# Performance work log

Measured on AMD Instinct MI355X. Metric: run time of the kernel, lower is better.

Reference implementation:

```python
import jax, jax.numpy as jnp
import numpy as np

T, H, E, I, K = 1024, 2048, 32, 1024, 2  # tokens, hidden, experts, intermediate (per rank), top_k


def setup_inputs() -> dict:
    key = jax.random.key(0)
    k0, k1, k2, k3 = jax.random.split(key, 4)
    s = 0.02  # weight init scale
    return {
        "hidden_states": jax.random.normal(k0, (T, H), jnp.float32),
        "w_qkv": jax.random.normal(k1, (3 * E, H), jnp.float32) * s,   # router query_key_value weight
        "w1": jax.random.normal(k2, (E, 2 * I, H), jnp.float32) * s,   # gate/up projection per expert
        "w2": jax.random.normal(k3, (E, H, I), jnp.float32) * s,       # down projection per expert
    }


def _router_logits(x, w_qkv):
    # ParallelAttention_router: per-token attention over the expert axis.
    mix = x @ w_qkv.T                      # [T, 3E]
    q, k, v = jnp.split(mix, 3, axis=-1)   # each [T, E]
    q = q.astype(jnp.float32)
    k = k.astype(jnp.float32)
    v = v.astype(jnp.float32)
    # attn[t, e, f] = softmax_f(q[t, e] * k[t, f])
    attn = jax.nn.softmax(q[:, :, None] * k[:, None, :], axis=-1)  # [T, E, E]
    return jnp.einsum('tef,tf->te', attn, v)                        # [T, E]


def reference(hidden_states, w_qkv, w1, w2):
    n_tok = hidden_states.shape[0]
    logits = _router_logits(hidden_states, w_qkv)                   # [T, E]
    top_logits, topk_ids = jax.lax.top_k(logits, K)                 # [T, K]
    topk_w = jax.nn.softmax(top_logits.astype(jnp.float32), axis=-1)  # renormalize=False -> plain softmax over top-k
    # Dense combine weights: zero for non-selected experts (honors top-k sparsity in math).
    combine = jnp.zeros((n_tok, E), jnp.float32).at[
        jnp.arange(n_tok)[:, None], topk_ids].add(topk_w)           # [T, E]
    # Expert MLP: SiLU-gated FFN (fused_experts contract: w1 -> [gate; up], w2 -> down).
    gate_up = jnp.einsum('th,eih->tei', hidden_states, w1)          # [T, E, 2I]
    gate, up = jnp.split(gate_up, 2, axis=-1)                       # each [T, E, I]
    h = jax.nn.silu(gate) * up * combine[:, :, None]                # fold combine weight in early
    out = jnp.einsum('tei,ehi->th', h, w2)                          # [T, H]
    return out.astype(hidden_states.dtype)
```

## Files before the change

### kernel.cpp

```cpp
#include <hip/hip_runtime.h>
#include <hip/hip_bf16.h>
#include <math.h>

#define TT 1024
#define HH 2048
#define EE 32
#define II 1024
#define BK2 128
#define SA2 136
#define TS2 (128 * SA2)
#define KSP 32
#define MB 64

typedef __attribute__((ext_vector_type(8))) short bf16x8;
typedef __attribute__((ext_vector_type(8))) unsigned short ushort8;
typedef __attribute__((ext_vector_type(4))) float f32x4;

__device__ __forceinline__ unsigned short f2b(float f) {
    union { float f; unsigned u; } c; c.f = f;
    unsigned r = c.u + 0x7FFFu + ((c.u >> 16) & 1u);
    return (unsigned short)(r >> 16);
}
__device__ __forceinline__ float b2f(unsigned short u) {
    union { unsigned u; float f; } c; c.u = ((unsigned)u) << 16;
    return c.f;
}
__device__ __forceinline__ unsigned cvtpk(float lo, float hi) {
    unsigned r;
    asm("v_cvt_pk_bf16_f32 %0, %1, %2" : "=v"(r) : "v"(lo), "v"(hi));
    return r;
}
__device__ __forceinline__ ushort8 pack8(float4 a, float4 b) {
    union { unsigned u[4]; ushort8 s; } cv;
    cv.u[0] = cvtpk(a.x, a.y); cv.u[1] = cvtpk(a.z, a.w);
    cv.u[2] = cvtpk(b.x, b.y); cv.u[3] = cvtpk(b.z, b.w);
    return cv.s;
}

__global__ __launch_bounds__(256) void k_mix(const float* __restrict__ x,
                                             const float* __restrict__ wqkv,
                                             float* __restrict__ mixp,
                                             unsigned short* __restrict__ xb) {
    __shared__ float xs[MB][68];
    __shared__ float ws_[96][68];
    const int tm0 = blockIdx.x * MB;
    const int k0 = blockIdx.y * 64;
    const int tid = threadIdx.x;
#pragma unroll
    for (int q = 0; q < 4; ++q) {
        int p = tid + q * 256;
        int row = p >> 4, c4 = (p & 15) * 4;
        *(float4*)&xs[row][c4] = *(const float4*)(x + (size_t)(tm0 + row) * HH + k0 + c4);
    }
#pragma unroll
    for (int q = 0; q < 6; ++q) {
        int p = tid + q * 256;
        int row = p >> 4, c4 = (p & 15) * 4;
        *(float4*)&ws_[row][c4] = *(const float4*)(wqkv + (size_t)row * HH + k0 + c4);
    }
    __syncthreads();
#pragma unroll
    for (int q = 0; q < 2; ++q) {
        int p = tid + q * 256;
        int row = p >> 3, c8 = (p & 7) * 8;
        float4 lo = *(const float4*)&xs[row][c8];
        float4 hi = *(const float4*)&xs[row][c8 + 4];
        *(ushort8*)(xb + (size_t)(tm0 + row) * HH + k0 + c8) = pack8(lo, hi);
    }
    const int tg = tid >> 4, cg = tid & 15;
    float acc[4][6];
#pragma unroll
    for (int i = 0; i < 4; ++i)
#pragma unroll
        for (int c = 0; c < 6; ++c) acc[i][c] = 0.f;
    for (int k = 0; k < 64; k += 4) {
        float4 xv[4], wv[6];
#pragma unroll
        for (int i = 0; i < 4; ++i) xv[i] = *(const float4*)&xs[tg * 4 + i][k];
#pragma unroll
        for (int c = 0; c < 6; ++c) wv[c] = *(const float4*)&ws_[cg * 6 + c][k];
#pragma unroll
        for (int i = 0; i < 4; ++i)
#pragma unroll
            for (int c = 0; c < 6; ++c)
                acc[i][c] += xv[i].x * wv[c].x + xv[i].y * wv[c].y +
                             xv[i].z * wv[c].z + xv[i].w * wv[c].w;
    }
    float* dst = mixp + ((size_t)blockIdx.y * TT + tm0) * 96;
#pragma unroll
    for (int i = 0; i < 4; ++i)
#pragma unroll
        for (int c = 0; c < 6; ++c)
            dst[(tg * 4 + i) * 96 + cg * 6 + c] = acc[i][c];
}

__global__ void k_router_attn(const float* __restrict__ mixp,
                              int* __restrict__ cnt,
                              int* __restrict__ tok_list,
                              float* __restrict__ wgt_list) {
    const int t = blockIdx.x;
    __shared__ float mrow[96];
    __shared__ float lg[EE];
    const int tid = threadIdx.x;
    if (tid < 96) {
        float s = 0.f;
        for (int sp = 0; sp < KSP; ++sp)
            s += mixp[((size_t)sp * TT + t) * 96 + tid];
        mrow[tid] = s;
    }
    __syncthreads();
    if (tid < EE) {
        float q = mrow[tid];
        float m = -1e30f;
        for (int f = 0; f < EE; ++f) m = fmaxf(m, q * mrow[32 + f]);
        float s = 0.f, a = 0.f;
        for (int f = 0; f < EE; ++f) {
            float ex = expf(q * mrow[32 + f] - m);
            s += ex;
            a += ex * mrow[64 + f];
        }
        lg[tid] = a / s;
    }
    __syncthreads();
    if (tid == 0) {
        int b0 = 0; float v0 = lg[0];
        for (int e2 = 1; e2 < EE; ++e2)
            if (lg[e2] > v0) { v0 = lg[e2]; b0 = e2; }
        int b1 = -1; float v1 = -1e30f;
        for (int e2 = 0; e2 < EE; ++e2)
            if (e2 != b0 && lg[e2] > v1) { v1 = lg[e2]; b1 = e2; }
        float ex = expf(v1 - v0);
        float w0 = 1.f / (1.f + ex);
        float w1 = ex / (1.f + ex);
        int p0 = atomicAdd(&cnt[b0], 1);
        tok_list[b0 * TT + p0] = t * 2 + 0;
        wgt_list[b0 * TT + p0] = w0;
        int p1 = atomicAdd(&cnt[b1], 1);
        tok_list[b1 * TT + p1] = t * 2 + 1;
        wgt_list[b1 * TT + p1] = w1;
    }
}

__global__ __launch_bounds__(256, 2) void k_gemm1(
    const unsigned short* __restrict__ xb, const float* __restrict__ w1,
    const int* __restrict__ cnt, const int* __restrict__ tok_list,
    const float* __restrict__ wgt_list, unsigned short* __restrict__ act) {
    const int e = blockIdx.y;
    const int M = cnt[e];
    const int m0 = blockIdx.z * 128;
    if (m0 >= M) return;
    const int i0 = blockIdx.x * 64;

    __shared__ __align__(16) unsigned short As[TS2];
    __shared__ __align__(16) unsigned short Bs[TS2];
    __shared__ int ts[128];
    __shared__ float tw[128];

    const int tid = threadIdx.x;
    if (tid < 128) {
        int mr = m0 + tid;
        if (mr < M) {
            ts[tid] = tok_list[e * TT + mr];
            tw[tid] = wgt_list[e * TT + mr];
        } else { ts[tid] = -1; tw[tid] = 0.f; }
    }
    __syncthreads();

    const float* w1e = w1 + (size_t)e * (2 * II) * HH;
    const int wid = tid >> 6;
    const int lane = tid & 63;
    const int wm = wid >> 1, wn = wid & 1;
    const int fr = lane & 15;
    const int kg = lane >> 4;
    const int srow = tid >> 4;
    const int sc8 = (tid & 15) * 8;

    f32x4 acc[4][4];
#pragma unroll
    for (int i = 0; i < 4; ++i)
#pragma unroll
        for (int j = 0; j < 4; ++j) acc[i][j] = (f32x4){0.f, 0.f, 0.f, 0.f};

    ushort8 pa8[8];
    float4 pb[16];
    const ushort8 u8z = {0, 0, 0, 0, 0, 0, 0, 0};

#define G1_LOAD(kk)                                                              \
    do {                                                                         \
        const int kkv_ = (kk);                                                   \
        _Pragma("unroll")                                                        \
        for (int q = 0; q < 8; ++q) {                                            \
            int row = q * 16 + srow;                                             \
            int entry = ts[row];                                                 \
            pa8[q] = (entry >= 0)                                                \
                ? *(const ushort8*)(xb + (size_t)(entry >> 1) * HH + kkv_ + sc8) \
                : u8z;                                                           \
            int brow = (row < 64) ? (i0 + row) : (II + i0 + row - 64);           \
            const float* gpb_ = w1e + (size_t)brow * HH + kkv_ + sc8;            \
            pb[2 * q] = ((const float4*)gpb_)[0];                                \
            pb[2 * q + 1] = ((const float4*)gpb_)[1];                            \
        }                                                                        \
    } while (0)

#define G1_CVT()                                                                 \
    do {                                                                         \
        _Pragma("unroll")                                                        \
        for (int q = 0; q < 8; ++q) {                                            \
            int row = q * 16 + srow;                                             \
            *(ushort8*)&As[row * SA2 + sc8] = pa8[q];                            \
            *(ushort8*)&Bs[row * SA2 + sc8] = pack8(pb[2 * q], pb[2 * q + 1]);   \
        }                                                                        \
    } while (0)

    const int NS = HH / BK2;
    G1_LOAD(0);
    for (int s = 0; s < NS; ++s) {
        __syncthreads();
        G1_CVT();
        __syncthreads();
        if (s + 1 < NS) G1_LOAD((s + 1) * BK2);
#pragma unroll
        for (int kh = 0; kh < 4; ++kh) {
            const int kb = kh * 32 + kg * 8;
            bf16x8 a[4], b[4];
#pragma unroll
            for (int i = 0; i < 4; ++i)
                a[i] = *(const bf16x8*)&As[(wm * 64 + i * 16 + fr) * SA2 + kb];
#pragma unroll
            for (int j = 0; j < 4; ++j)
                b[j] = *(const bf16x8*)&Bs[(wn * 64 + j * 16 + fr) * SA2 + kb];
#pragma unroll
            for (int i = 0; i < 4; ++i)
#pragma unroll
                for (int j = 0; j < 4; ++j)
                    acc[i][j] = __builtin_amdgcn_mfma_f32_16x16x32_bf16(a[i], b[j], acc[i][j], 0, 0, 0);
        }
    }
#undef G1_LOAD
#undef G1_CVT

    unsigned short* upls = As;
    __syncthreads();
    if (wn == 1) {
#pragma unroll
        for (int mi = 0; mi < 4; ++mi)
#pragma unroll
            for (int reg = 0; reg < 4; ++reg) {
                int mrow = wm * 64 + mi * 16 + kg * 4 + reg;
#pragma unroll
                for (int ni = 0; ni < 4; ++ni)
                    upls[mrow * 64 + ni * 16 + fr] = f2b(acc[mi][ni][reg]);
            }
    }
    __syncthreads();
    if (wn == 0) {
#pragma unroll
        for (int mi = 0; mi < 4; ++mi)
#pragma unroll
            for (int reg = 0; reg < 4; ++reg) {
                int mrow = wm * 64 + mi * 16 + kg * 4 + reg;
                int entry = ts[mrow];
                if (entry < 0) continue;
                float w = tw[mrow];
                unsigned short* dst = act + (size_t)entry * II + i0;
#pragma unroll
                for (int ni = 0; ni < 4; ++ni) {
                    float g = acc[mi][ni][reg];
                    float u = b2f(upls[mrow * 64 + ni * 16 + fr]);
                    dst[ni * 16 + fr] = f2b((g / (1.f + __expf(-g))) * u * w);
                }
            }
    }
}

__global__ __launch_bounds__(256, 2) void k_gemm2(
    const unsigned short* __restrict__ act, const float* __restrict__ w2,
    const int* __restrict__ cnt, const int* __restrict__ tok_list,
    float* __restrict__ out) {
    const int e = blockIdx.y;
    const int M = cnt[e];
    const int m0 = blockIdx.z * 128;
    if (m0 >= M) return;
    const int n0 = blockIdx.x * 128;

    __shared__ __align__(16) unsigned short As[TS2];
    __shared__ __align__(16) unsigned short Bs[TS2];
    __shared__ int ts[128];

    const int tid = threadIdx.x;
    if (tid < 128) {
        int mr = m0 + tid;
        ts[tid] = (mr < M) ? tok_list[e * TT + mr] : -1;
    }
    __syncthreads();

    const float* w2e = w2 + (size_t)e * HH * II;
    const int wid = tid >> 6;
    const int lane = tid & 63;
    const int wm = wid >> 1, wn = wid & 1;
    const int fr = lane & 15;
    const int kg = lane >> 4;
    const int srow = tid >> 4;
    const int sc8 = (tid & 15) * 8;

    f32x4 acc[4][4];
#pragma unroll
    for (int i = 0; i < 4; ++i)
#pragma unroll
        for (int j = 0; j < 4; ++j) acc[i][j] = (f32x4){0.f, 0.f, 0.f, 0.f};

    ushort8 pa8[8];
    float4 pb[16];
    const ushort8 u8z = {0, 0, 0, 0, 0, 0, 0, 0};

#define G2_LOAD(kk)                                                              \
    do {                                                                         \
        const int kkv_ = (kk);                                                   \
        _Pragma("unroll")                                                        \
        for (int q = 0; q < 8; ++q) {                                            \
            int row = q * 16 + srow;                                             \
            int entry = ts[row];                                                 \
            pa8[q] = (entry >= 0)                                                \
                ? *(const ushort8*)(act + (size_t)entry * II + kkv_ + sc8)       \
                : u8z;                                                           \
            const float* gpb_ = w2e + (size_t)(n0 + row) * II + kkv_ + sc8;      \
            pb[2 * q] = ((const float4*)gpb_)[0];                                \
            pb[2 * q + 1] = ((const float4*)gpb_)[1];                            \
        }                                                                        \
    } while (0)

#define G2_CVT()                                                                 \
    do {                                                                         \
        _Pragma("unroll")                                                        \
        for (int q = 0; q < 8; ++q) {                                            \
            int row = q * 16 + srow;                                             \
            *(ushort8*)&As[row * SA2 + sc8] = pa8[q];                            \
            *(ushort8*)&Bs[row * SA2 + sc8] = pack8(pb[2 * q], pb[2 * q + 1]);   \
        }                                                                        \
    } while (0)

    const int NS = II / BK2;
    G2_LOAD(0);
    for (int s = 0; s < NS; ++s) {
        __syncthreads();
        G2_CVT();
        __syncthreads();
        if (s + 1 < NS) G2_LOAD((s + 1) * BK2);
#pragma unroll
        for (int kh = 0; kh < 4; ++kh) {
            const int kb = kh * 32 + kg * 8;
            bf16x8 a[4], b[4];
#pragma unroll
            for (int i = 0; i < 4; ++i)
                a[i] = *(const bf16x8*)&As[(wm * 64 + i * 16 + fr) * SA2 + kb];
#pragma unroll
            for (int j = 0; j < 4; ++j)
                b[j] = *(const bf16x8*)&Bs[(wn * 64 + j * 16 + fr) * SA2 + kb];
#pragma unroll
            for (int i = 0; i < 4; ++i)
#pragma unroll
                for (int j = 0; j < 4; ++j)
                    acc[i][j] = __builtin_amdgcn_mfma_f32_16x16x32_bf16(a[i], b[j], acc[i][j], 0, 0, 0);
        }
    }
#undef G2_LOAD
#undef G2_CVT

#pragma unroll
    for (int mi = 0; mi < 4; ++mi) {
#pragma unroll
        for (int reg = 0; reg < 4; ++reg) {
            int m = wm * 64 + mi * 16 + kg * 4 + reg;
            int entry = ts[m];
            if (entry < 0) continue;
            int t = entry >> 1;
            float* op = out + (size_t)t * HH + n0 + wn * 64;
#pragma unroll
            for (int ni = 0; ni < 4; ++ni)
                atomicAdd(&op[ni * 16 + fr], acc[mi][ni][reg]);
        }
    }
}

extern "C" void kernel_launch(void* const* d_in, const int* in_sizes, int n_in,
                              void* d_out, int out_size, void* d_ws, size_t ws_size,
                              hipStream_t stream) {
    const float* x    = (const float*)d_in[0];
    const float* wqkv = (const float*)d_in[1];
    const float* w1   = (const float*)d_in[2];
    const float* w2   = (const float*)d_in[3];
    float* out = (float*)d_out;

    char* ws = (char*)d_ws;
    float* mixp           = (float*)(ws);
    float* wgt_list       = (float*)(ws + 12582912);
    int*   tok_list       = (int*)  (ws + 12713984);
    int*   cnt            = (int*)  (ws + 12845056);
    unsigned short* xb    = (unsigned short*)(ws + 12845184);
    unsigned short* act   = (unsigned short*)(ws + 17039488);

    (void)hipMemsetAsync(cnt, 0, 128, stream);
    (void)hipMemsetAsync(out, 0, (size_t)out_size * sizeof(float), stream);

    k_mix<<<dim3(TT / MB, KSP), 256, 0, stream>>>(x, wqkv, mixp, xb);
    k_router_attn<<<TT, 128, 0, stream>>>(mixp, cnt, tok_list, wgt_list);
    k_gemm1<<<dim3(II / 64, EE, 8), 256, 0, stream>>>(xb, w1, cnt, tok_list, wgt_list, act);
    k_gemm2<<<dim3(HH / 128, EE, 8), 256, 0, stream>>>(act, w2, cnt, tok_list, out);
}
```

Before: 218.5 us.

## Use 512-thread blocks with BK=256 K-tiles and 2x4 warp layout in expert GEMMs

Both expert GEMM kernels now launch 512 threads (8 waves arranged 2x4) instead of 256, and the K-tile per stage doubles from 128 to 256, halving the number of sync/convert stages. Each wave computes a 64x32 sub-tile, which cuts accumulator registers per thread and doubles the waves per block that can hide the fp32 weight-load latency. The trade-off is doubled LDS per block (about 135 KB), which likely drops occupancy to one block per CU, plus more LDS A-fragment re-reads per MFMA. The gate/up epilogue is remapped to the new wave layout.

After: 231.4 us. 5.9% more time.

```diff
diff --git a/kernel.cpp b/kernel.cpp
--- a/kernel.cpp
+++ b/kernel.cpp
@@ -6,9 +6,9 @@
 #define HH 2048
 #define EE 32
 #define II 1024
-#define BK2 128
-#define SA2 136
-#define TS2 (128 * SA2)
+#define BK3 256
+#define SA3 264
+#define TS3 (128 * SA3)
 #define KSP 32
 #define MB 64
 
@@ -141,7 +141,7 @@
     }
 }
 
-__global__ __launch_bounds__(256, 2) void k_gemm1(
+__global__ __launch_bounds__(512, 2) void k_gemm1(
     const unsigned short* __restrict__ xb, const float* __restrict__ w1,
     const int* __restrict__ cnt, const int* __restrict__ tok_list,
     const float* __restrict__ wgt_list, unsigned short* __restrict__ act) {
@@ -151,8 +151,8 @@
     if (m0 >= M) return;
     const int i0 = blockIdx.x * 64;
 
-    __shared__ __align__(16) unsigned short As[TS2];
-    __shared__ __align__(16) unsigned short Bs[TS2];
+    __shared__ __align__(16) unsigned short As[TS3];
+    __shared__ __align__(16) unsigned short Bs[TS3];
     __shared__ int ts[128];
     __shared__ float tw[128];
 
@@ -169,17 +169,17 @@
     const float* w1e = w1 + (size_t)e * (2 * II) * HH;
     const int wid = tid >> 6;
     const int lane = tid & 63;
-    const int wm = wid >> 1, wn = wid & 1;
+    const int wm = wid >> 2, wn = wid & 3;
     const int fr = lane & 15;
     const int kg = lane >> 4;
-    const int srow = tid >> 4;
-    const int sc8 = (tid & 15) * 8;
-
-    f32x4 acc[4][4];
+    const int srow = tid >> 5;
+    const int sc8 = (tid & 31) * 8;
+
+    f32x4 acc[4][2];
 #pragma unroll
     for (int i = 0; i < 4; ++i)
 #pragma unroll
-        for (int j = 0; j < 4; ++j) acc[i][j] = (f32x4){0.f, 0.f, 0.f, 0.f};
+        for (int j = 0; j < 2; ++j) acc[i][j] = (f32x4){0.f, 0.f, 0.f, 0.f};
 
     ushort8 pa8[8];
     float4 pb[16];
@@ -207,32 +207,32 @@
         _Pragma("unroll")                                                        \
         for (int q = 0; q < 8; ++q) {                                            \
             int row = q * 16 + srow;                                             \
-            *(ushort8*)&As[row * SA2 + sc8] = pa8[q];                            \
-            *(ushort8*)&Bs[row * SA2 + sc8] = pack8(pb[2 * q], pb[2 * q + 1]);   \
+            *(ushort8*)&As[row * SA3 + sc8] = pa8[q];                            \
+            *(ushort8*)&Bs[row * SA3 + sc8] = pack8(pb[2 * q], pb[2 * q + 1]);   \
         }                                                                        \
     } while (0)
 
-    const int NS = HH / BK2;
+    const int NS = HH / BK3;
     G1_LOAD(0);
     for (int s = 0; s < NS; ++s) {
         __syncthreads();
         G1_CVT();
         __syncthreads();
-        if (s + 1 < NS) G1_LOAD((s + 1) * BK2);
-#pragma unroll
-        for (int kh = 0; kh < 4; ++kh) {
+        if (s + 1 < NS) G1_LOAD((s + 1) * BK3);
+#pragma unroll
+        for (int kh = 0; kh < 8; ++kh) {
             const int kb = kh * 32 + kg * 8;
-            bf16x8 a[4], b[4];
+            bf16x8 a[4], b[2];
 #pragma unroll
             for (int i = 0; i < 4; ++i)
-                a[i] = *(const bf16x8*)&As[(wm * 64 + i * 16 + fr) * SA2 + kb];
-#pragma unroll
-            for (int j = 0; j < 4; ++j)
-                b[j] = *(const bf16x8*)&Bs[(wn * 64 + j * 16 + fr) * SA2 + kb];
+                a[i] = *(const bf16x8*)&As[(wm * 64 + i * 16 + fr) * SA3 + kb];
+#pragma unroll
+            for (int j = 0; j < 2; ++j)
+                b[j] = *(const bf16x8*)&Bs[(wn * 32 + j * 16 + fr) * SA3 + kb];
 #pragma unroll
             for (int i = 0; i < 4; ++i)
 #pragma unroll
-                for (int j = 0; j < 4; ++j)
+                for (int j = 0; j < 2; ++j)
                     acc[i][j] = __builtin_amdgcn_mfma_f32_16x16x32_bf16(a[i], b[j], acc[i][j], 0, 0, 0);
         }
     }
@@ -241,39 +241,42 @@
 
     unsigned short* upls = As;
     __syncthreads();
-    if (wn == 1) {
+    if (wn >= 2) {
 #pragma unroll
         for (int mi = 0; mi < 4; ++mi)
 #pragma unroll
             for (int reg = 0; reg < 4; ++reg) {
-                int mrow = wm * 64 + mi * 16 + kg * 4 + reg;
-#pragma unroll
-                for (int ni = 0; ni < 4; ++ni)
-                    upls[mrow * 64 + ni * 16 + fr] = f2b(acc[mi][ni][reg]);
-            }
-    }
-    __syncthreads();
-    if (wn == 0) {
-#pragma unroll
-        for (int mi = 0; mi < 4; ++mi)
-#pragma unroll
-            for (int reg = 0; reg < 4; ++reg) {
-                int mrow = wm * 64 + mi * 16 + kg * 4 + reg;
-                int entry = ts[mrow];
-                if (entry < 0) continue;
-                float w = tw[mrow];
-                unsigned short* dst = act + (size_t)entry * II + i0;
-#pragma unroll
-                for (int ni = 0; ni < 4; ++ni) {
-                    float g = acc[mi][ni][reg];
-                    float u = b2f(upls[mrow * 64 + ni * 16 + fr]);
-                    dst[ni * 16 + fr] = f2b((g / (1.f + __expf(-g))) * u * w);
+                int m = wm * 64 + mi * 16 + kg * 4 + reg;
+#pragma unroll
+                for (int j = 0; j < 2; ++j) {
+                    int un = (wn - 2) * 32 + j * 16 + fr;
+                    upls[m * 64 + un] = f2b(acc[mi][j][reg]);
                 }
             }
     }
-}
-
-__global__ __launch_bounds__(256, 2) void k_gemm2(
+    __syncthreads();
+    if (wn < 2) {
+#pragma unroll
+        for (int mi = 0; mi < 4; ++mi)
+#pragma unroll
+            for (int reg = 0; reg < 4; ++reg) {
+                int m = wm * 64 + mi * 16 + kg * 4 + reg;
+                int entry = ts[m];
+                if (entry < 0) continue;
+                float w = tw[m];
+                unsigned short* dst = act + (size_t)entry * II + i0;
+#pragma unroll
+                for (int j = 0; j < 2; ++j) {
+                    int n = wn * 32 + j * 16 + fr;
+                    float g = acc[mi][j][reg];
+                    float u = b2f(upls[m * 64 + n]);
+                    dst[n] = f2b((g / (1.f + __expf(-g))) * u * w);
+                }
+            }
+    }
+}
+
+__global__ __launch_bounds__(512, 2) void k_gemm2(
     const unsigned short* __restrict__ act, const float* __restrict__ w2,
     const int* __restrict__ cnt, const int* __restrict__ tok_list,
     float* __restrict__ out) {
@@ -283,8 +286,8 @@
     if (m0 >= M) return;
     const int n0 = blockIdx.x * 128;
 
-    __shared__ __align__(16) unsigned short As[TS2];
-    __shared__ __align__(16) unsigned short Bs[TS2];
+    __shared__ __align__(16) unsigned short As[TS3];
+    __shared__ __align__(16) unsigned short Bs[TS3];
     __shared__ int ts[128];
 
     const int tid = threadIdx.x;
@@ -297,17 +300,17 @@
     const float* w2e = w2 + (size_t)e * HH * II;
     const int wid = tid >> 6;
     const int lane = tid & 63;
-    const int wm = wid >> 1, wn = wid & 1;
+    const int wm = wid >> 2, wn = wid & 3;
     const int fr = lane & 15;
     const int kg = lane >> 4;
-    const int srow = tid >> 4;
-    const int sc8 = (tid & 15) * 8;
-
-    f32x4 acc[4][4];
+    const int srow = tid >> 5;
+    const int sc8 = (tid & 31) * 8;
+
+    f32x4 acc[4][2];
 #pragma unroll
     for (int i = 0; i < 4; ++i)
 #pragma unroll
-        for (int j = 0; j < 4; ++j) acc[i][j] = (f32x4){0.f, 0.f, 0.f, 0.f};
+        for (int j = 0; j < 2; ++j) acc[i][j] = (f32x4){0.f, 0.f, 0.f, 0.f};
 
     ushort8 pa8[8];
     float4 pb[16];
@@ -334,32 +337,32 @@
         _Pragma("unroll")                                                        \
         for (int q = 0; q < 8; ++q) {                                            \
             int row = q * 16 + srow;                                             \
-            *(ushort8*)&As[row * SA2 + sc8] = pa8[q];                            \
-            *(ushort8*)&Bs[row * SA2 + sc8] = pack8(pb[2 * q], pb[2 * q + 1]);   \
+            *(ushort8*)&As[row * SA3 + sc8] = pa8[q];                            \
+            *(ushort8*)&Bs[row * SA3 + sc8] = pack8(pb[2 * q], pb[2 * q + 1]);   \
         }                                                                        \
     } while (0)
 
-    const int NS = II / BK2;
+    const int NS = II / BK3;
     G2_LOAD(0);
     for (int s = 0; s < NS; ++s) {
         __syncthreads();
         G2_CVT();
         __syncthreads();
-        if (s + 1 < NS) G2_LOAD((s + 1) * BK2);
-#pragma unroll
-        for (int kh = 0; kh < 4; ++kh) {
+        if (s + 1 < NS) G2_LOAD((s + 1) * BK3);
+#pragma unroll
+        for (int kh = 0; kh < 8; ++kh) {
             const int kb = kh * 32 + kg * 8;
-            bf16x8 a[4], b[4];
+            bf16x8 a[4], b[2];
 #pragma unroll
             for (int i = 0; i < 4; ++i)
-                a[i] = *(const bf16x8*)&As[(wm * 64 + i * 16 + fr) * SA2 + kb];
-#pragma unroll
-            for (int j = 0; j < 4; ++j)
-                b[j] = *(const bf16x8*)&Bs[(wn * 64 + j * 16 + fr) * SA2 + kb];
+                a[i] = *(const bf16x8*)&As[(wm * 64 + i * 16 + fr) * SA3 + kb];
+#pragma unroll
+            for (int j = 0; j < 2; ++j)
+                b[j] = *(const bf16x8*)&Bs[(wn * 32 + j * 16 + fr) * SA3 + kb];
 #pragma unroll
             for (int i = 0; i < 4; ++i)
 #pragma unroll
-                for (int j = 0; j < 4; ++j)
+                for (int j = 0; j < 2; ++j)
                     acc[i][j] = __builtin_amdgcn_mfma_f32_16x16x32_bf16(a[i], b[j], acc[i][j], 0, 0, 0);
         }
     }
@@ -374,10 +377,12 @@
             int entry = ts[m];
             if (entry < 0) continue;
             int t = entry >> 1;
-            float* op = out + (size_t)t * HH + n0 + wn * 64;
-#pragma unroll
-            for (int ni = 0; ni < 4; ++ni)
-                atomicAdd(&op[ni * 16 + fr], acc[mi][ni][reg]);
+            float* op = out + (size_t)t * HH + n0;
+#pragma unroll
+            for (int j = 0; j < 2; ++j) {
+                int n = wn * 32 + j * 16 + fr;
+                atomicAdd(&op[n], acc[mi][j][reg]);
+            }
         }
     }
 }
@@ -404,6 +409,6 @@
 
     k_mix<<<dim3(TT / MB, KSP), 256, 0, stream>>>(x, wqkv, mixp, xb);
     k_router_attn<<<TT, 128, 0, stream>>>(mixp, cnt, tok_list, wgt_list);
-    k_gemm1<<<dim3(II / 64, EE, 8), 256, 0, stream>>>(xb, w1, cnt, tok_list, wgt_list, act);
-    k_gemm2<<<dim3(HH / 128, EE, 8), 256, 0, stream>>>(act, w2, cnt, tok_list, out);
-}
+    k_gemm1<<<dim3(II / 64, EE, 8), 512, 0, stream>>>(xb, w1, cnt, tok_list, wgt_list, act);
+    k_gemm2<<<dim3(HH / 128, EE, 8), 512, 0, stream>>>(act, w2, cnt, tok_list, out);
+}
```
